# Kernel tuning notes

Hardware: AMD Instinct MI355X
Metric: run time of the kernel (lower is better)

Reference implementation:

```python
import jax, jax.numpy as jnp
import numpy as np

B, M, C = 32, 64, 36
INPUT_DIM, HIDDEN, N_CLASS = 1024, 512, 1000
NEG_INF = -1e10


def setup_inputs() -> dict:
    key = jax.random.key(0)
    ks = jax.random.split(key, 16)
    s = 0.02
    return {
        "mention_embeddings": jax.random.normal(ks[0], (B, M, INPUT_DIM), jnp.float32),
        "class_labels": jax.random.uniform(ks[1], (B, C, N_CLASS), jnp.float32),
        "mention_mask": jnp.ones((B, M), jnp.float32),
        "class_mask": jnp.ones((B, C), jnp.float32),
        # visual_embedder: Linear(n_class, H) -> ReLU -> Linear(H, H)
        "vw1": jax.random.normal(ks[2], (N_CLASS, HIDDEN), jnp.float32) * s,
        "vb1": jnp.zeros((HIDDEN,), jnp.float32),
        "vw2": jax.random.normal(ks[3], (HIDDEN, HIDDEN), jnp.float32) * s,
        "vb2": jnp.zeros((HIDDEN,), jnp.float32),
        # mention_embedder: Linear(input_dim, H) -> ReLU -> Linear(H, H)
        "mw1": jax.random.normal(ks[4], (INPUT_DIM, HIDDEN), jnp.float32) * s,
        "mb1": jnp.zeros((HIDDEN,), jnp.float32),
        "mw2": jax.random.normal(ks[5], (HIDDEN, HIDDEN), jnp.float32) * s,
        "mb2": jnp.zeros((HIDDEN,), jnp.float32),
        # attention: Linear(H, H) -> ReLU -> Linear(H, 1)
        "aw1": jax.random.normal(ks[6], (HIDDEN, HIDDEN), jnp.float32) * s,
        "ab1": jnp.zeros((HIDDEN,), jnp.float32),
        "aw2": jax.random.normal(ks[7], (HIDDEN, 1), jnp.float32) * s,
        "ab2": jnp.zeros((1,), jnp.float32),
    }


def reference(mention_embeddings, class_labels, mention_mask, class_mask,
              vw1, vb1, vw2, vb2, mw1, mb1, mw2, mb2, aw1, ab1, aw2, ab2):
    # visual embeddings: (B, C, H)
    vis = jax.nn.relu(class_labels @ vw1 + vb1) @ vw2 + vb2
    # mention embeddings: (B, M, H)
    men = jax.nn.relu(mention_embeddings @ mw1 + mb1) @ mw2 + mb2
    # broadcast outer product: (B, M, C, H)
    prod = men[:, :, None, :] * vis[:, None, :, :]
    # 2-layer MLP attention score -> (B, M, C)
    h = jax.nn.relu(prod @ aw1 + ab1)
    attn = (h @ aw2 + ab2)[..., 0]
    # masking
    attn = attn * mention_mask[:, :, None] * class_mask[:, None, :]
    attn = jnp.where(attn != 0, attn, NEG_INF)
    return attn
```

## Files before the change

kernel.cpp:

```cpp
#include <hip/hip_runtime.h>

typedef _Float16 f16;
typedef _Float16 f16x8 __attribute__((ext_vector_type(8)));
typedef _Float16 f16x4 __attribute__((ext_vector_type(4)));
typedef float f32x4 __attribute__((ext_vector_type(4)));
typedef float fl4 __attribute__((ext_vector_type(4)));

#define NEG_INF_F (-1e10f)

__device__ __forceinline__ void stage16(const f16* g, f16* l) {
    __builtin_amdgcn_global_load_lds((const __attribute__((address_space(1))) void*)g,
                                     (__attribute__((address_space(3))) void*)l, 16, 0, 0);
}

__global__ __launch_bounds__(256) void prep2(const float* __restrict__ me,
                                             const float* __restrict__ mw1,
                                             const float* __restrict__ vw1,
                                             const float* __restrict__ mw2,
                                             const float* __restrict__ vw2,
                                             const float* __restrict__ aw1,
                                             const float* __restrict__ cl,
                                             f16* __restrict__ me_h,
                                             f16* __restrict__ mw1t, f16* __restrict__ vw1t,
                                             f16* __restrict__ mw2t, f16* __restrict__ vw2t,
                                             f16* __restrict__ aw1t, f16* __restrict__ cl_h) {
    int bx = blockIdx.x, t = threadIdx.x;
    if (bx < 1792) {
        __shared__ float tile[32][33];
        const float* src; f16* dst; int Ksrc, Kp, tid;
        if (bx < 512)       { src = mw1; dst = mw1t; Ksrc = 1024; Kp = 1024; tid = bx; }
        else if (bx < 1024) { src = vw1; dst = vw1t; Ksrc = 1000; Kp = 1024; tid = bx - 512; }
        else if (bx < 1280) { src = mw2; dst = mw2t; Ksrc = 512;  Kp = 512;  tid = bx - 1024; }
        else if (bx < 1536) { src = vw2; dst = vw2t; Ksrc = 512;  Kp = 512;  tid = bx - 1280; }
        else                { src = aw1; dst = aw1t; Ksrc = 512;  Kp = 512;  tid = bx - 1536; }
        int tk = tid >> 4, tn = tid & 15;
        int x = t & 31, y = t >> 5;
        #pragma unroll
        for (int r = 0; r < 4; r++) {
            int k = tk * 32 + y * 4 + r;
            tile[y * 4 + r][x] = (k < Ksrc) ? src[k * 512 + tn * 32 + x] : 0.f;
        }
        __syncthreads();
        #pragma unroll
        for (int r = 0; r < 4; r++) {
            int n = tn * 32 + y * 4 + r;
            dst[n * Kp + tk * 32 + x] = (f16)tile[x][y * 4 + r];
        }
        return;
    }
    if (bx < 3840) {
        int i = (bx - 1792) * 256 + t;
        fl4 v = *(const fl4*)(me + i * 4);
        f16x4 h;
        #pragma unroll
        for (int e = 0; e < 4; e++) h[e] = (f16)v[e];
        *(f16x4*)(me_h + i * 4) = h;
        return;
    }
    {
        int i = (bx - 3840) * 256 + t;
        int idx = i * 4;
        int r = idx >> 10, k0 = idx & 1023;
        f16x4 h;
        if (k0 < 1000) {
            fl4 v = *(const fl4*)(cl + r * 1000 + k0);
            #pragma unroll
            for (int e = 0; e < 4; e++) h[e] = (f16)v[e];
        } else {
            #pragma unroll
            for (int e = 0; e < 4; e++) h[e] = (f16)0.f;
        }
        *(f16x4*)(cl_h + idx) = h;
    }
}

__global__ __launch_bounds__(256, 4) void gemm_stg3(const f16* __restrict__ Am,
                                                    const f16* __restrict__ Av,
                                                    const f16* __restrict__ Wm,
                                                    const f16* __restrict__ Wv,
                                                    const float* __restrict__ bm,
                                                    const float* __restrict__ bv,
                                                    f16* __restrict__ om,
                                                    f16* __restrict__ ov,
                                                    int K, int relu) {
    __shared__ f16 ab[4][2048], bb[4][2048];

    int t = threadIdx.x, lane = t & 63, w = t >> 6;
    int rl = lane & 15, kg = lane >> 4;
    int mq = w & 1, nq = w >> 1;
    bool isv = blockIdx.x >= 32;
    int mb = isv ? blockIdx.x - 32 : blockIdx.x;
    const f16* A = isv ? Av : Am;
    const f16* Wt = isv ? Wv : Wm;
    const float* bias = isv ? bv : bm;
    f16* out = isv ? ov : om;
    int m0 = mb * 64, n0 = blockIdx.y * 64;
    int pu = kg ^ ((rl >> 1) & 3);

    int srow = t >> 2;
    int sk8 = (t & 3) ^ ((srow >> 1) & 3);
    const f16* a_src = A + (m0 + srow) * K + sk8 * 8;
    const f16* b_src = Wt + (n0 + srow) * K + sk8 * 8;
    int ndbl = K >> 6;

    f32x4 acc[2][2] = {};

    stage16(a_src, &ab[0][t * 8]);
    stage16(b_src, &bb[0][t * 8]);
    stage16(a_src + 32, &ab[1][t * 8]);
    stage16(b_src + 32, &bb[1][t * 8]);
    __syncthreads();

    for (int ss = 0; ss < ndbl; ss++) {
        if (ss + 1 < ndbl) {
            int ka = (ss * 2 + 2) * 32, kb = (ss * 2 + 3) * 32;
            stage16(a_src + ka, &ab[(ss * 2 + 2) & 3][t * 8]);
            stage16(b_src + ka, &bb[(ss * 2 + 2) & 3][t * 8]);
            stage16(a_src + kb, &ab[(ss * 2 + 3) & 3][t * 8]);
            stage16(b_src + kb, &bb[(ss * 2 + 3) & 3][t * 8]);
        }
        #pragma unroll
        for (int h = 0; h < 2; h++) {
            int cur = (ss * 2 + h) & 3;
            f16x8 af[2], bf[2];
            #pragma unroll
            for (int f = 0; f < 2; f++) {
                af[f] = *(const f16x8*)&ab[cur][((mq * 32 + f * 16 + rl) * 4 + pu) * 8];
                bf[f] = *(const f16x8*)&bb[cur][((nq * 32 + f * 16 + rl) * 4 + pu) * 8];
            }
            #pragma unroll
            for (int fi = 0; fi < 2; fi++)
                #pragma unroll
                for (int fj = 0; fj < 2; fj++)
                    acc[fi][fj] = __builtin_amdgcn_mfma_f32_16x16x32_f16(af[fi], bf[fj], acc[fi][fj], 0, 0, 0);
        }
        __syncthreads();
    }

    #pragma unroll
    for (int fi = 0; fi < 2; fi++)
        #pragma unroll
        for (int fj = 0; fj < 2; fj++) {
            int col = n0 + nq * 32 + fj * 16 + rl;
            float bv2 = bias[col];
            #pragma unroll
            for (int r = 0; r < 4; r++) {
                int row = m0 + mq * 32 + fi * 16 + kg * 4 + r;
                float v = acc[fi][fj][r] + bv2;
                if (relu) v = fmaxf(v, 0.f);
                out[row * 512 + col] = (f16)v;
            }
        }
}

__global__ __launch_bounds__(256, 2) void attn_f19(const f16* __restrict__ men,
                                                   const f16* __restrict__ vis,
                                                   const f16* __restrict__ aw1t,
                                                   const float* __restrict__ ab1,
                                                   const float* __restrict__ aw2,
                                                   float* __restrict__ partial) {
    __shared__ f16 awb[4][4096];
    __shared__ f16 mnb[4][2048];
    __shared__ f16 vist[2048];
    __shared__ float red[2][4][64];

    int t = threadIdx.x, lane = t & 63, w = t >> 6;
    int mh = w & 1, jq = w >> 1;
    int cq = blockIdx.x, jh = blockIdx.y, b = blockIdx.z;
    int c0 = cq * 4;
    int rl = lane & 15, kg = lane >> 4;
    int pu = kg ^ ((rl >> 1) & 3);

    int srow = t >> 2;
    int sk8 = (t & 3) ^ ((srow >> 1) & 3);
    const f16* aw_src = aw1t + (jh * 128 + srow) * 512 + sk8 * 8;
    const f16* mn_src = men + (b * 64 + srow) * 512 + sk8 * 8;
    const f16* vi_src = vis + (b * 36 + c0 + (t >> 6)) * 512 + (t & 63) * 8;

    f32x4 acc[4][2][4] = {};

    stage16(vi_src, &vist[t * 8]);
    #pragma unroll
    for (int bt = 0; bt < 3; bt++) {
        stage16(aw_src + bt * 32, &awb[bt][t * 8]);
        stage16(aw_src + 64 * 512 + bt * 32, &awb[bt][2048 + t * 8]);
        stage16(mn_src + bt * 32, &mnb[bt][t * 8]);
    }
    asm volatile("s_waitcnt vmcnt(3)" ::: "memory");
    __builtin_amdgcn_s_barrier();
    __builtin_amdgcn_sched_barrier(0);

    f16x8 cmm[2], cbf[4], cvv[4];
    #pragma unroll
    for (int fi = 0; fi < 2; fi++)
        cmm[fi] = *(const f16x8*)&mnb[0][((mh * 32 + fi * 16 + rl) * 4 + pu) * 8];
    #pragma unroll
    for (int fj = 0; fj < 4; fj++)
        cbf[fj] = *(const f16x8*)&awb[0][((jq * 64 + fj * 16 + rl) * 4 + pu) * 8];
    #pragma unroll
    for (int c = 0; c < 4; c++)
        cvv[c] = *(const f16x8*)&vist[c * 512 + kg * 8];
    __builtin_amdgcn_sched_barrier(0);

    #pragma unroll
    for (int s = 0; s < 16; s++) {
        if (s > 0) {
            if (s >= 14) asm volatile("s_waitcnt vmcnt(0)" ::: "memory");
            else         asm volatile("s_waitcnt vmcnt(3)" ::: "memory");
            __builtin_amdgcn_s_barrier();
            __builtin_amdgcn_sched_barrier(0);
        }
        if (s <= 12) {
            int k3 = (s + 3) * 32;
            int nb = (s + 3) & 3;
            stage16(aw_src + k3, &awb[nb][t * 8]);
            stage16(aw_src + 64 * 512 + k3, &awb[nb][2048 + t * 8]);
            stage16(mn_src + k3, &mnb[nb][t * 8]);
        }

        #pragma unroll
        for (int fi = 0; fi < 2; fi++)
            #pragma unroll
            for (int c = 0; c < 4; c++) {
                f16x8 a = cmm[fi] * cvv[c];
                #pragma unroll
                for (int fj = 0; fj < 4; fj++)
                    acc[c][fi][fj] = __builtin_amdgcn_mfma_f32_16x16x32_f16(a, cbf[fj], acc[c][fi][fj], 0, 0, 0);
            }

        if (s < 15) {
            const int nx = (s + 1) & 3;
            f16x8 nmm[2], nbf[4], nvv[4];
            #pragma unroll
            for (int fi = 0; fi < 2; fi++)
                nmm[fi] = *(const f16x8*)&mnb[nx][((mh * 32 + fi * 16 + rl) * 4 + pu) * 8];
            #pragma unroll
            for (int fj = 0; fj < 4; fj++)
                nbf[fj] = *(const f16x8*)&awb[nx][((jq * 64 + fj * 16 + rl) * 4 + pu) * 8];
            #pragma unroll
            for (int c = 0; c < 4; c++)
                nvv[c] = *(const f16x8*)&vist[c * 512 + (s + 1) * 32 + kg * 8];
            __builtin_amdgcn_sched_barrier(0);
            #pragma unroll
            for (int fi = 0; fi < 2; fi++) cmm[fi] = nmm[fi];
            #pragma unroll
            for (int fj = 0; fj < 4; fj++) cbf[fj] = nbf[fj];
            #pragma unroll
            for (int c = 0; c < 4; c++) cvv[c] = nvv[c];
        }
    }

    int j0 = jh * 128 + jq * 64;
    float ab1v[4], aw2v[4];
    #pragma unroll
    for (int fj = 0; fj < 4; fj++) {
        int j = j0 + fj * 16 + rl;
        ab1v[fj] = ab1[j];
        aw2v[fj] = aw2[j];
    }
    #pragma unroll
    for (int c = 0; c < 4; c++) {
        float part[2][4];
        #pragma unroll
        for (int fi = 0; fi < 2; fi++)
            #pragma unroll
            for (int r = 0; r < 4; r++) {
                float sv = 0.f;
                #pragma unroll
                for (int fj = 0; fj < 4; fj++)
                    sv += fmaxf(acc[c][fi][fj][r] + ab1v[fj], 0.f) * aw2v[fj];
                part[fi][r] = sv;
            }
        #pragma unroll
        for (int mask = 1; mask < 16; mask <<= 1)
            #pragma unroll
            for (int fi = 0; fi < 2; fi++)
                #pragma unroll
                for (int r = 0; r < 4; r++)
                    part[fi][r] += __shfl_xor(part[fi][r], mask);
        float myv = 0.f;
        #pragma unroll
        for (int fi = 0; fi < 2; fi++)
            #pragma unroll
            for (int r = 0; r < 4; r++)
                myv = (rl == fi * 4 + r) ? part[fi][r] : myv;
        if (rl < 8) {
            int m = mh * 32 + (rl >> 2) * 16 + kg * 4 + (rl & 3);
            red[jq][c][m] = myv;
        }
    }
    __syncthreads();

    if (t < 256) {
        int ci = t >> 6, m = t & 63;
        float s = red[0][ci][m] + red[1][ci][m];
        partial[((jh * 32 + b) * 64 + m) * 36 + c0 + ci] = s;
    }
}

__global__ __launch_bounds__(256) void postproc(const float* __restrict__ partial,
                                                const float* __restrict__ mm,
                                                const float* __restrict__ cm,
                                                const float* __restrict__ ab2,
                                                float* __restrict__ out) {
    int i = blockIdx.x * 256 + threadIdx.x;
    int b = i / 2304;
    int rest = i - b * 2304;
    int m = rest / 36, c = rest - m * 36;
    float s = 0.f;
    #pragma unroll
    for (int jh = 0; jh < 4; jh++)
        s += partial[((jh * 32 + b) * 64 + m) * 36 + c];
    float v = (s + ab2[0]) * mm[b * 64 + m] * cm[b * 36 + c];
    out[i] = (v != 0.f) ? v : NEG_INF_F;
}

extern "C" void kernel_launch(void* const* d_in, const int* in_sizes, int n_in,
                              void* d_out, int out_size, void* d_ws, size_t ws_size,
                              hipStream_t stream) {
    const float* ME  = (const float*)d_in[0];
    const float* CL  = (const float*)d_in[1];
    const float* MM  = (const float*)d_in[2];
    const float* CM  = (const float*)d_in[3];
    const float* VW1 = (const float*)d_in[4];
    const float* VB1 = (const float*)d_in[5];
    const float* VW2 = (const float*)d_in[6];
    const float* VB2 = (const float*)d_in[7];
    const float* MW1 = (const float*)d_in[8];
    const float* MB1 = (const float*)d_in[9];
    const float* MW2 = (const float*)d_in[10];
    const float* MB2 = (const float*)d_in[11];
    const float* AW1 = (const float*)d_in[12];
    const float* AB1 = (const float*)d_in[13];
    const float* AW2 = (const float*)d_in[14];
    const float* AB2 = (const float*)d_in[15];
    float* out = (float*)d_out;

    char* ws = (char*)d_ws;
    f16* me_h  = (f16*)ws; ws += (size_t)2048 * 1024 * 2;
    f16* cl_h  = (f16*)ws; ws += (size_t)1152 * 1024 * 2;
    f16* mw1t  = (f16*)ws; ws += (size_t)512 * 1024 * 2;
    f16* vw1t  = (f16*)ws; ws += (size_t)512 * 1024 * 2;
    f16* mw2t  = (f16*)ws; ws += (size_t)512 * 512 * 2;
    f16* vw2t  = (f16*)ws; ws += (size_t)512 * 512 * 2;
    f16* aw1t  = (f16*)ws; ws += (size_t)512 * 512 * 2;
    f16* men1  = (f16*)ws; ws += (size_t)2048 * 512 * 2;
    f16* menh  = (f16*)ws; ws += (size_t)2048 * 512 * 2;
    f16* vis1  = (f16*)ws; ws += (size_t)1152 * 512 * 2;
    f16* vish  = (f16*)ws; ws += (size_t)1152 * 512 * 2;
    float* part = (float*)ws; ws += (size_t)4 * 32 * 64 * 36 * 4;

    prep2<<<4992, 256, 0, stream>>>(ME, MW1, VW1, MW2, VW2, AW1, CL,
                                    me_h, mw1t, vw1t, mw2t, vw2t, aw1t, cl_h);
    gemm_stg3<<<dim3(50, 8), 256, 0, stream>>>(me_h, cl_h, mw1t, vw1t, MB1, VB1,
                                               men1, vis1, 1024, 1);
    gemm_stg3<<<dim3(50, 8), 256, 0, stream>>>(men1, vis1, mw2t, vw2t, MB2, VB2,
                                               menh, vish, 512, 0);
    attn_f19<<<dim3(9, 4, 32), 256, 0, stream>>>(menh, vish, aw1t, AB1, AW2, part);
    postproc<<<288, 256, 0, stream>>>(part, MM, CM, AB2, out);
}
```

Measured before the change: 74.39 us.

## Deepen GEMM pipeline to three-stage prefetch with register double-buffered fragments

The two small MLP GEMMs now stage three 32-wide K slices ahead into a 4-slot LDS ring. Instead of a full __syncthreads per pair of steps, each step waits on vmcnt and issues a raw s_barrier. LDS fragments for the next step are loaded into registers while the current MFMAs run, to hide LDS and global latency. This raises register pressure and depends on hand-placed waitcnt and sched_barrier ordering being correct.

```diff
diff --git a/kernel.cpp b/kernel.cpp
--- a/kernel.cpp
+++ b/kernel.cpp
@@ -74,7 +74,7 @@
     }
 }
 
-__global__ __launch_bounds__(256, 4) void gemm_stg3(const f16* __restrict__ Am,
+__global__ __launch_bounds__(256, 4) void gemm_stg4(const f16* __restrict__ Am,
                                                     const f16* __restrict__ Av,
                                                     const f16* __restrict__ Wm,
                                                     const f16* __restrict__ Wv,
@@ -101,40 +101,59 @@
     int sk8 = (t & 3) ^ ((srow >> 1) & 3);
     const f16* a_src = A + (m0 + srow) * K + sk8 * 8;
     const f16* b_src = Wt + (n0 + srow) * K + sk8 * 8;
-    int ndbl = K >> 6;
+    int nsteps = K >> 5;
 
     f32x4 acc[2][2] = {};
 
-    stage16(a_src, &ab[0][t * 8]);
-    stage16(b_src, &bb[0][t * 8]);
-    stage16(a_src + 32, &ab[1][t * 8]);
-    stage16(b_src + 32, &bb[1][t * 8]);
-    __syncthreads();
-
-    for (int ss = 0; ss < ndbl; ss++) {
-        if (ss + 1 < ndbl) {
-            int ka = (ss * 2 + 2) * 32, kb = (ss * 2 + 3) * 32;
-            stage16(a_src + ka, &ab[(ss * 2 + 2) & 3][t * 8]);
-            stage16(b_src + ka, &bb[(ss * 2 + 2) & 3][t * 8]);
-            stage16(a_src + kb, &ab[(ss * 2 + 3) & 3][t * 8]);
-            stage16(b_src + kb, &bb[(ss * 2 + 3) & 3][t * 8]);
-        }
-        #pragma unroll
-        for (int h = 0; h < 2; h++) {
-            int cur = (ss * 2 + h) & 3;
-            f16x8 af[2], bf[2];
+    #pragma unroll
+    for (int bt = 0; bt < 3; bt++) {
+        stage16(a_src + bt * 32, &ab[bt][t * 8]);
+        stage16(b_src + bt * 32, &bb[bt][t * 8]);
+    }
+    asm volatile("s_waitcnt vmcnt(2)" ::: "memory");
+    __builtin_amdgcn_s_barrier();
+    __builtin_amdgcn_sched_barrier(0);
+
+    f16x8 caf[2], cbf[2];
+    #pragma unroll
+    for (int f = 0; f < 2; f++) {
+        caf[f] = *(const f16x8*)&ab[0][((mq * 32 + f * 16 + rl) * 4 + pu) * 8];
+        cbf[f] = *(const f16x8*)&bb[0][((nq * 32 + f * 16 + rl) * 4 + pu) * 8];
+    }
+    __builtin_amdgcn_sched_barrier(0);
+
+    for (int s = 0; s < nsteps; s++) {
+        if (s > 0) {
+            if (s >= nsteps - 2) asm volatile("s_waitcnt vmcnt(0)" ::: "memory");
+            else                 asm volatile("s_waitcnt vmcnt(2)" ::: "memory");
+            __builtin_amdgcn_s_barrier();
+            __builtin_amdgcn_sched_barrier(0);
+        }
+        if (s + 3 < nsteps) {
+            int k3 = (s + 3) * 32;
+            int nb = (s + 3) & 3;
+            stage16(a_src + k3, &ab[nb][t * 8]);
+            stage16(b_src + k3, &bb[nb][t * 8]);
+        }
+
+        #pragma unroll
+        for (int fi = 0; fi < 2; fi++)
+            #pragma unroll
+            for (int fj = 0; fj < 2; fj++)
+                acc[fi][fj] = __builtin_amdgcn_mfma_f32_16x16x32_f16(caf[fi], cbf[fj], acc[fi][fj], 0, 0, 0);
+
+        if (s + 1 < nsteps) {
+            const int nx = (s + 1) & 3;
+            f16x8 naf[2], nbf[2];
             #pragma unroll
             for (int f = 0; f < 2; f++) {
-                af[f] = *(const f16x8*)&ab[cur][((mq * 32 + f * 16 + rl) * 4 + pu) * 8];
-                bf[f] = *(const f16x8*)&bb[cur][((nq * 32 + f * 16 + rl) * 4 + pu) * 8];
+                naf[f] = *(const f16x8*)&ab[nx][((mq * 32 + f * 16 + rl) * 4 + pu) * 8];
+                nbf[f] = *(const f16x8*)&bb[nx][((nq * 32 + f * 16 + rl) * 4 + pu) * 8];
             }
-            #pragma unroll
-            for (int fi = 0; fi < 2; fi++)
-                #pragma unroll
-                for (int fj = 0; fj < 2; fj++)
-                    acc[fi][fj] = __builtin_amdgcn_mfma_f32_16x16x32_f16(af[fi], bf[fj], acc[fi][fj], 0, 0, 0);
-        }
-        __syncthreads();
+            __builtin_amdgcn_sched_barrier(0);
+            #pragma unroll
+            for (int f = 0; f < 2; f++) { caf[f] = naf[f]; cbf[f] = nbf[f]; }
+        }
     }
 
     #pragma unroll
@@ -352,9 +371,9 @@
 
     prep2<<<4992, 256, 0, stream>>>(ME, MW1, VW1, MW2, VW2, AW1, CL,
                                     me_h, mw1t, vw1t, mw2t, vw2t, aw1t, cl_h);
-    gemm_stg3<<<dim3(50, 8), 256, 0, stream>>>(me_h, cl_h, mw1t, vw1t, MB1, VB1,
+    gemm_stg4<<<dim3(50, 8), 256, 0, stream>>>(me_h, cl_h, mw1t, vw1t, MB1, VB1,
                                                men1, vis1, 1024, 1);
-    gemm_stg3<<<dim3(50, 8), 256, 0, stream>>>(men1, vis1, mw2t, vw2t, MB2, VB2,
+    gemm_stg4<<<dim3(50, 8), 256, 0, stream>>>(men1, vis1, mw2t, vw2t, MB2, VB2,
                                                menh, vish, 512, 0);
     attn_f19<<<dim3(9, 4, 32), 256, 0, stream>>>(menh, vish, aw1t, AB1, AW2, part);
     postproc<<<288, 256, 0, stream>>>(part, MM, CM, AB2, out);
```

Result: slower. 76.53 us (+2.9%).
